# Kernel tuning notes

Hardware: AMD Instinct MI355X
Metric: run time of the kernel (lower is better)

## Reference

```python
import jax, jax.numpy as jnp
import numpy as np

B, S, D, H = 2, 2048, 1024, 16
HD = D // H
SCALE = HD ** -0.5


def setup_inputs() -> dict:
    key = jax.random.key(0)
    ks = jax.random.split(key, 9)
    w = 0.02
    return {
        "query": jax.random.normal(ks[0], (B, S, D), jnp.float32),
        "key": jax.random.normal(ks[1], (B, S, D), jnp.float32),
        "value": jax.random.normal(ks[2], (B, S, D), jnp.float32),
        # precomputed structural bias matrix B_struct [B, S, S]
        "bias_struct": jax.random.uniform(ks[3], (B, S, S), jnp.float32, 0.0, 1.5),
        "Wq": jax.random.normal(ks[4], (D, D), jnp.float32) * w,
        "bq": jnp.zeros((D,), jnp.float32),
        "Wk": jax.random.normal(ks[5], (D, D), jnp.float32) * w,
        "bk": jnp.zeros((D,), jnp.float32),
        "Wv": jax.random.normal(ks[6], (D, D), jnp.float32) * w,
        "bv": jnp.zeros((D,), jnp.float32),
        "Wo": jax.random.normal(ks[7], (D, D), jnp.float32) * w,
        "bo": jnp.zeros((D,), jnp.float32),
        "lambda_bias": jnp.array(1.0, jnp.float32),
    }


def _split_heads(x):
    # [B, S, D] -> [B, H, S, HD]
    b, s, _ = x.shape
    return x.reshape(b, s, H, HD).transpose(0, 2, 1, 3)


def reference(query, key, value, bias_struct, Wq, bq, Wk, bk, Wv, bv, Wo, bo, lambda_bias):
    # Linear projections (torch Linear: x @ W.T + b)
    Q = _split_heads(query @ Wq.T + bq)
    K = _split_heads(key @ Wk.T + bk)
    V = _split_heads(value @ Wv.T + bv)
    # scores = QK^T * scale + lambda * B_struct (broadcast over heads)
    scores = jnp.einsum("bhqd,bhkd->bhqk", Q, K) * SCALE
    scores = scores + lambda_bias * bias_struct[:, None, :, :]
    attn = jax.nn.softmax(scores, axis=-1)
    out = jnp.einsum("bhqk,bhkd->bhqd", attn, V)
    out = out.transpose(0, 2, 1, 3).reshape(query.shape[0], query.shape[1], D)
    return out @ Wo.T + bo
```

## Files before the change

kernel.cpp:

```cpp
#include <hip/hip_runtime.h>
#include <hip/hip_bf16.h>

namespace {

constexpr int B  = 2;
constexpr int S  = 2048;
constexpr int D  = 1024;
constexpr int H  = 16;
constexpr float SCALE = 0.125f;

constexpr int GM = B * S;
constexpr int GN = D;
constexpr int GK = D;

typedef __bf16 bf16x8 __attribute__((ext_vector_type(8)));
typedef float  f32x4  __attribute__((ext_vector_type(4)));
typedef unsigned short u16;
typedef u16 u16x8 __attribute__((ext_vector_type(8)));
typedef u16 u16x4 __attribute__((ext_vector_type(4)));

__device__ __forceinline__ u16 f2bf(float f) {
  union { float f; unsigned u; } v{f};
  unsigned r = v.u + 0x7fffu + ((v.u >> 16) & 1u);
  return (u16)(r >> 16);
}

__device__ __forceinline__ f32x4 mfma16(bf16x8 a, bf16x8 b, f32x4 c) {
  return __builtin_amdgcn_mfma_f32_16x16x32_bf16(a, b, c, 0, 0, 0);
}

__device__ __forceinline__ void gload_lds16(const u16* g, u16* l) {
  __builtin_amdgcn_global_load_lds(
      (const __attribute__((address_space(1))) void*)g,
      (__attribute__((address_space(3))) void*)l, 16, 0, 0);
}

__global__ __launch_bounds__(256) void cvt3_k(
    const float* __restrict__ a, const float* __restrict__ b,
    const float* __restrict__ c, u16* __restrict__ da,
    u16* __restrict__ db, u16* __restrict__ dc)
{
  const float* s = (blockIdx.z == 0) ? a : (blockIdx.z == 1) ? b : c;
  u16* d = (blockIdx.z == 0) ? da : (blockIdx.z == 1) ? db : dc;
  size_t i = ((size_t)blockIdx.x * 256 + threadIdx.x) * 4;
  float4 v = *(const float4*)&s[i];
  u16x4 o = { f2bf(v.x), f2bf(v.y), f2bf(v.z), f2bf(v.w) };
  *(u16x4*)&d[i] = o;
}

__global__ __launch_bounds__(256) void cvt4_k(
    const float* __restrict__ a, const float* __restrict__ b,
    const float* __restrict__ c, const float* __restrict__ e,
    u16* __restrict__ da, u16* __restrict__ db,
    u16* __restrict__ dc, u16* __restrict__ de)
{
  const float* s = (blockIdx.z == 0) ? a : (blockIdx.z == 1) ? b
                 : (blockIdx.z == 2) ? c : e;
  u16* d = (blockIdx.z == 0) ? da : (blockIdx.z == 1) ? db
         : (blockIdx.z == 2) ? dc : de;
  size_t i = ((size_t)blockIdx.x * 256 + threadIdx.x) * 4;
  float4 v = *(const float4*)&s[i];
  u16x4 o = { f2bf(v.x), f2bf(v.y), f2bf(v.z), f2bf(v.w) };
  *(u16x4*)&d[i] = o;
}

template <bool OUTBF, int NZ>
__global__ __launch_bounds__(256) void gemm128_k(
    const u16* __restrict__ A0, const u16* __restrict__ W0, const float* __restrict__ bias0,
    const u16* __restrict__ A1, const u16* __restrict__ W1, const float* __restrict__ bias1,
    u16* __restrict__ Cb0, u16* __restrict__ Cb1, float* __restrict__ Cf)
{
  __shared__ u16 Al[2][128 * 64];
  __shared__ u16 Bl[2][128 * 64];

  const int z = (NZ > 1) ? blockIdx.z : 0;
  const u16* Ap = (z == 0) ? A0 : A1;
  const u16* Wp = (z == 0) ? W0 : W1;
  const float* bias = (z == 0) ? bias0 : bias1;
  u16* Cb = (z == 0) ? Cb0 : Cb1;

  const int tid  = threadIdx.x;
  const int lane = tid & 63;
  const int w    = tid >> 6;
  const int wr = w >> 1, wc = w & 1;
  const int lg = lane >> 4, ll = lane & 15;
  const int bm = blockIdx.y * 128, bn = blockIdx.x * 128;

  auto STAGE = [&](int buf, int k0) {
#pragma unroll
    for (int i = 0; i < 4; ++i) {
      const int c   = (w * 4 + i) * 64 + lane;
      const int row = c >> 3, cs = c & 7;
      const int dofs = ((cs * 16) ^ ((row & 7) << 4)) >> 1;
      gload_lds16(&Ap[(size_t)(bm + row) * GK + k0 + dofs],
                  &Al[buf][(w * 4 + i) * 512]);
      gload_lds16(&Wp[(size_t)(bn + row) * GK + k0 + dofs],
                  &Bl[buf][(w * 4 + i) * 512]);
    }
  };

  f32x4 acc[4][4] = {};

  STAGE(0, 0);
  __syncthreads();

  int cur = 0;
  constexpr int NT = GK / 64;
  for (int t = 0; t < NT; ++t) {
    if (t + 1 < NT) STAGE(cur ^ 1, (t + 1) * 64);
#pragma unroll
    for (int half = 0; half < 2; ++half) {
      bf16x8 af[4], bfr[4];
#pragma unroll
      for (int mi = 0; mi < 4; ++mi) {
        const int row = wr * 64 + mi * 16 + ll;
        af[mi] = *(const bf16x8*)&Al[cur][row * 64 +
                   (((half * 64 + lg * 16) ^ ((row & 7) << 4)) >> 1)];
      }
#pragma unroll
      for (int ni = 0; ni < 4; ++ni) {
        const int row = wc * 64 + ni * 16 + ll;
        bfr[ni] = *(const bf16x8*)&Bl[cur][row * 64 +
                   (((half * 64 + lg * 16) ^ ((row & 7) << 4)) >> 1)];
      }
#pragma unroll
      for (int mi = 0; mi < 4; ++mi)
#pragma unroll
        for (int ni = 0; ni < 4; ++ni)
          acc[mi][ni] = mfma16(af[mi], bfr[ni], acc[mi][ni]);
    }
    __syncthreads();
    cur ^= 1;
  }

#pragma unroll
  for (int ni = 0; ni < 4; ++ni) {
    const int gcol = bn + wc * 64 + ni * 16 + ll;
    const float bv = bias[gcol];
#pragma unroll
    for (int mi = 0; mi < 4; ++mi) {
      const int grow = bm + wr * 64 + mi * 16 + lg * 4;
#pragma unroll
      for (int r = 0; r < 4; ++r) {
        float v = acc[mi][ni][r] + bv;
        if (OUTBF) Cb[(size_t)(grow + r) * GN + gcol] = f2bf(v);
        else       Cf[(size_t)(grow + r) * GN + gcol] = v;
      }
    }
  }
}

__global__ __launch_bounds__(256) void transpose_v_k(
    const u16* __restrict__ Vb, u16* __restrict__ Vt)
{
  __shared__ u16 T[64][72];
  const int tid = threadIdx.x;
  const int bh = blockIdx.y, b = bh >> 4, h = bh & 15;
  const int s0 = blockIdx.x * 64;
#pragma unroll
  for (int it = 0; it < 2; ++it) {
    int idx = tid + it * 256;
    int s = idx >> 3, dc = idx & 7;
    *(uint4*)&T[s][dc * 8] =
        *(const uint4*)&Vb[(size_t)(b * S + s0 + s) * D + h * 64 + dc * 8];
  }
  __syncthreads();
#pragma unroll
  for (int it = 0; it < 2; ++it) {
    int idx = tid + it * 256;
    int d = idx >> 3, sc = idx & 7;
    u16x8 o;
#pragma unroll
    for (int jj = 0; jj < 8; ++jj) o[jj] = T[sc * 8 + jj][d];
    *(u16x8*)&Vt[((size_t)bh * 64 + d) * S + s0 + sc * 8] = o;
  }
}

__global__ __launch_bounds__(256, 3) void attn_mfma2_k(
    const u16* __restrict__ Qb, const u16* __restrict__ Kb,
    const u16* __restrict__ Vt, const float* __restrict__ biasS,
    const float* __restrict__ lamp, u16* __restrict__ Ob)
{
  __shared__ u16 Kl[2][64 * 64];
  __shared__ u16 Pl[4][16][72];

  const int tid  = threadIdx.x;
  const int lane = tid & 63;
  const int w    = tid >> 6;
  const int lg = lane >> 4, ll = lane & 15;
  const int bh = blockIdx.y, b = bh >> 4, h = bh & 15;
  const int qw = blockIdx.x * 64 + w * 16;
  const float lam = lamp[0];

  bf16x8 aQ[2];
  {
    const u16* qrow = &Qb[(size_t)(b * S + qw + ll) * D + h * 64];
    aQ[0] = *(const bf16x8*)&qrow[lg * 8];
    aQ[1] = *(const bf16x8*)&qrow[32 + lg * 8];
  }

  const u16* Kbase = &Kb[(size_t)(b * S) * D + h * 64];
  const u16* Vbase = &Vt[(size_t)bh * 64 * S];
  const float* Bb  = &biasS[((size_t)b * S + qw + lg * 4) * S];

  auto STAGE_K = [&](int buf, int k0) {
#pragma unroll
    for (int i = 0; i < 2; ++i) {
      const int c   = (w * 2 + i) * 64 + lane;
      const int row = c >> 3, cs = c & 7;
      const int dofs = ((cs * 16) ^ ((row & 7) << 4)) >> 1;
      gload_lds16(&Kbase[(size_t)(k0 + row) * D + dofs],
                  &Kl[buf][(w * 2 + i) * 512]);
    }
  };

  f32x4 accO[4] = {};
  float m_r[4], l_r[4];
#pragma unroll
  for (int r = 0; r < 4; ++r) { m_r[r] = -1e30f; l_r[r] = 0.f; }

  float bc[4][4];
  STAGE_K(0, 0);
#pragma unroll
  for (int r = 0; r < 4; ++r)
#pragma unroll
    for (int kf = 0; kf < 4; ++kf)
      bc[r][kf] = Bb[(size_t)r * S + kf * 16 + ll];
  __syncthreads();

  int cur = 0;
  constexpr int NT = S / 64;
  for (int t = 0; t < NT; ++t) {
    const int k0 = t * 64;
    if (t + 1 < NT) STAGE_K(cur ^ 1, k0 + 64);

    bf16x8 v0[4], v1[4];
#pragma unroll
    for (int nf = 0; nf < 4; ++nf) {
      const u16* vrow = &Vbase[(size_t)(nf * 16 + ll) * S + k0];
      v0[nf] = *(const bf16x8*)&vrow[lg * 8];
      v1[nf] = *(const bf16x8*)&vrow[32 + lg * 8];
    }
    float bn[4][4];
    if (t + 1 < NT) {
#pragma unroll
      for (int r = 0; r < 4; ++r)
#pragma unroll
        for (int kf = 0; kf < 4; ++kf)
          bn[r][kf] = Bb[(size_t)r * S + k0 + 64 + kf * 16 + ll];
    }

    f32x4 sf[4];
#pragma unroll
    for (int kf = 0; kf < 4; ++kf) {
      const int row = kf * 16 + ll;
      const u16* kr = &Kl[cur][row * 64];
      bf16x8 kb0 = *(const bf16x8*)&kr[((lg * 16) ^ ((row & 7) << 4)) >> 1];
      bf16x8 kb1 = *(const bf16x8*)&kr[((64 + lg * 16) ^ ((row & 7) << 4)) >> 1];
      f32x4 t4 = {0.f, 0.f, 0.f, 0.f};
      t4 = mfma16(aQ[0], kb0, t4);
      t4 = mfma16(aQ[1], kb1, t4);
#pragma unroll
      for (int r = 0; r < 4; ++r)
        t4[r] = t4[r] * SCALE + lam * bc[r][kf];
      sf[kf] = t4;
    }

#pragma unroll
    for (int r = 0; r < 4; ++r) {
      float pm = fmaxf(fmaxf(sf[0][r], sf[1][r]), fmaxf(sf[2][r], sf[3][r]));
      pm = fmaxf(pm, __shfl_xor(pm, 1));
      pm = fmaxf(pm, __shfl_xor(pm, 2));
      pm = fmaxf(pm, __shfl_xor(pm, 4));
      pm = fmaxf(pm, __shfl_xor(pm, 8));
      float nm = fmaxf(m_r[r], pm);
      float cf = __expf(m_r[r] - nm);
      m_r[r] = nm;
      float ps = 0.f;
#pragma unroll
      for (int kf = 0; kf < 4; ++kf) {
        float p = __expf(sf[kf][r] - nm);
        Pl[w][lg * 4 + r][kf * 16 + ll] = f2bf(p);
        ps += p;
      }
      ps += __shfl_xor(ps, 1);
      ps += __shfl_xor(ps, 2);
      ps += __shfl_xor(ps, 4);
      ps += __shfl_xor(ps, 8);
      l_r[r] = l_r[r] * cf + ps;
#pragma unroll
      for (int nf = 0; nf < 4; ++nf) accO[nf][r] *= cf;
    }

    bf16x8 aP0 = *(const bf16x8*)&Pl[w][ll][lg * 8];
    bf16x8 aP1 = *(const bf16x8*)&Pl[w][ll][32 + lg * 8];
#pragma unroll
    for (int nf = 0; nf < 4; ++nf) {
      accO[nf] = mfma16(aP0, v0[nf], accO[nf]);
      accO[nf] = mfma16(aP1, v1[nf], accO[nf]);
    }

    if (t + 1 < NT) {
#pragma unroll
      for (int r = 0; r < 4; ++r)
#pragma unroll
        for (int kf = 0; kf < 4; ++kf) bc[r][kf] = bn[r][kf];
    }
    __syncthreads();
    cur ^= 1;
  }

  float inv[4];
#pragma unroll
  for (int r = 0; r < 4; ++r) inv[r] = 1.0f / l_r[r];
#pragma unroll
  for (int nf = 0; nf < 4; ++nf)
#pragma unroll
    for (int r = 0; r < 4; ++r)
      Ob[(size_t)(b * S + qw + lg * 4 + r) * D + h * 64 + nf * 16 + ll] =
          f2bf(accO[nf][r] * inv[r]);
}

}

extern "C" void kernel_launch(void* const* d_in, const int* in_sizes, int n_in,
                              void* d_out, int out_size, void* d_ws, size_t ws_size,
                              hipStream_t stream)
{
  const float* query = (const float*)d_in[0];
  const float* key   = (const float*)d_in[1];
  const float* value = (const float*)d_in[2];
  const float* biasS = (const float*)d_in[3];
  const float* Wq = (const float*)d_in[4];
  const float* bq = (const float*)d_in[5];
  const float* Wk = (const float*)d_in[6];
  const float* bk = (const float*)d_in[7];
  const float* Wv = (const float*)d_in[8];
  const float* bv = (const float*)d_in[9];
  const float* Wo = (const float*)d_in[10];
  const float* bo = (const float*)d_in[11];
  const float* lam = (const float*)d_in[12];
  float* out = (float*)d_out;

  char* ws = (char*)d_ws;
  const size_t MB = 1024 * 1024;
  u16* Xq  = (u16*)(ws + 0 * MB);
  u16* Xk  = (u16*)(ws + 8 * MB);
  u16* Xv  = (u16*)(ws + 16 * MB);
  u16* WqB = (u16*)(ws + 24 * MB);
  u16* WkB = (u16*)(ws + 26 * MB);
  u16* WvB = (u16*)(ws + 28 * MB);
  u16* WoB = (u16*)(ws + 30 * MB);
  u16* Qbf = (u16*)(ws + 32 * MB);
  u16* Kbf = (u16*)(ws + 40 * MB);
  u16* Vbf = Xq;
  u16* Vt  = Xk;
  u16* Obf = Xv;

  cvt3_k<<<dim3(4096, 1, 3), 256, 0, stream>>>(query, key, value, Xq, Xk, Xv);
  cvt4_k<<<dim3(1024, 1, 4), 256, 0, stream>>>(Wq, Wk, Wv, Wo, WqB, WkB, WvB, WoB);

  dim3 pgrid(GN / 128, GM / 128, 2);
  gemm128_k<true, 2><<<pgrid, 256, 0, stream>>>(
      Xq, WqB, bq, Xk, WkB, bk, Qbf, Kbf, nullptr);
  dim3 vgrid(GN / 128, GM / 128, 1);
  gemm128_k<true, 1><<<vgrid, 256, 0, stream>>>(
      Xv, WvB, bv, nullptr, nullptr, nullptr, Vbf, nullptr, nullptr);

  transpose_v_k<<<dim3(S / 64, B * H), 256, 0, stream>>>(Vbf, Vt);

  attn_mfma2_k<<<dim3(S / 64, B * H), 256, 0, stream>>>(Qbf, Kbf, Vt, biasS, lam, Obf);

  gemm128_k<false, 1><<<vgrid, 256, 0, stream>>>(
      Obf, WoB, bo, nullptr, nullptr, nullptr, nullptr, nullptr, out);
}
```

Before: 364.1 us.

## Split attention over two KV halves with merge kernel; fuse QKV GEMMs

Result: slower. 888.5 us (+144.0%).

```diff
diff --git a/kernel.cpp b/kernel.cpp
--- a/kernel.cpp
+++ b/kernel.cpp
@@ -7,7 +7,9 @@
 constexpr int S  = 2048;
 constexpr int D  = 1024;
 constexpr int H  = 16;
+constexpr int BH = B * H;
 constexpr float SCALE = 0.125f;
+constexpr float THR = 8.0f;
 
 constexpr int GM = B * S;
 constexpr int GN = D;
@@ -23,6 +25,10 @@
   union { float f; unsigned u; } v{f};
   unsigned r = v.u + 0x7fffu + ((v.u >> 16) & 1u);
   return (u16)(r >> 16);
+}
+__device__ __forceinline__ float bf2f(u16 u) {
+  union { unsigned u; float f; } v{(unsigned)u << 16};
+  return v.f;
 }
 
 __device__ __forceinline__ f32x4 mfma16(bf16x8 a, bf16x8 b, f32x4 c) {
@@ -65,52 +71,59 @@
 }
 
 template <bool OUTBF, int NZ>
-__global__ __launch_bounds__(256) void gemm128_k(
-    const u16* __restrict__ A0, const u16* __restrict__ W0, const float* __restrict__ bias0,
-    const u16* __restrict__ A1, const u16* __restrict__ W1, const float* __restrict__ bias1,
-    u16* __restrict__ Cb0, u16* __restrict__ Cb1, float* __restrict__ Cf)
-{
-  __shared__ u16 Al[2][128 * 64];
-  __shared__ u16 Bl[2][128 * 64];
+__global__ __launch_bounds__(256) void gemm_k(
+    const u16* __restrict__ A0, const u16* __restrict__ A1, const u16* __restrict__ A2,
+    const u16* __restrict__ W0, const u16* __restrict__ W1, const u16* __restrict__ W2,
+    const float* __restrict__ b0, const float* __restrict__ b1, const float* __restrict__ b2,
+    u16* __restrict__ C0, u16* __restrict__ C1, u16* __restrict__ C2,
+    float* __restrict__ Cf)
+{
+  constexpr int BM = 128, BN = 64, BK = 64;
+  __shared__ u16 Al[2][BM * BK];
+  __shared__ u16 Bl[2][BN * BK];
 
   const int z = (NZ > 1) ? blockIdx.z : 0;
-  const u16* Ap = (z == 0) ? A0 : A1;
-  const u16* Wp = (z == 0) ? W0 : W1;
-  const float* bias = (z == 0) ? bias0 : bias1;
-  u16* Cb = (z == 0) ? Cb0 : Cb1;
+  const u16* Ap = (z == 0) ? A0 : (z == 1) ? A1 : A2;
+  const u16* Wp = (z == 0) ? W0 : (z == 1) ? W1 : W2;
+  const float* bias = (z == 0) ? b0 : (z == 1) ? b1 : b2;
+  u16* Cb = (z == 0) ? C0 : (z == 1) ? C1 : C2;
 
   const int tid  = threadIdx.x;
   const int lane = tid & 63;
   const int w    = tid >> 6;
   const int wr = w >> 1, wc = w & 1;
   const int lg = lane >> 4, ll = lane & 15;
-  const int bm = blockIdx.y * 128, bn = blockIdx.x * 128;
+  const int bm = blockIdx.y * BM, bn = blockIdx.x * BN;
 
   auto STAGE = [&](int buf, int k0) {
 #pragma unroll
     for (int i = 0; i < 4; ++i) {
-      const int c   = (w * 4 + i) * 64 + lane;
+      const int c = i * 256 + tid;
       const int row = c >> 3, cs = c & 7;
       const int dofs = ((cs * 16) ^ ((row & 7) << 4)) >> 1;
-      gload_lds16(&Ap[(size_t)(bm + row) * GK + k0 + dofs],
-                  &Al[buf][(w * 4 + i) * 512]);
-      gload_lds16(&Wp[(size_t)(bn + row) * GK + k0 + dofs],
-                  &Bl[buf][(w * 4 + i) * 512]);
+      gload_lds16(&Ap[(size_t)(bm + row) * GK + k0 + dofs], &Al[buf][c * 8]);
+    }
+#pragma unroll
+    for (int i = 0; i < 2; ++i) {
+      const int c = i * 256 + tid;
+      const int row = c >> 3, cs = c & 7;
+      const int dofs = ((cs * 16) ^ ((row & 7) << 4)) >> 1;
+      gload_lds16(&Wp[(size_t)(bn + row) * GK + k0 + dofs], &Bl[buf][c * 8]);
     }
   };
 
-  f32x4 acc[4][4] = {};
+  f32x4 acc[4][2] = {};
 
   STAGE(0, 0);
   __syncthreads();
 
   int cur = 0;
-  constexpr int NT = GK / 64;
+  constexpr int NT = GK / BK;
   for (int t = 0; t < NT; ++t) {
-    if (t + 1 < NT) STAGE(cur ^ 1, (t + 1) * 64);
+    if (t + 1 < NT) STAGE(cur ^ 1, (t + 1) * BK);
 #pragma unroll
     for (int half = 0; half < 2; ++half) {
-      bf16x8 af[4], bfr[4];
+      bf16x8 af[4], bfr[2];
 #pragma unroll
       for (int mi = 0; mi < 4; ++mi) {
         const int row = wr * 64 + mi * 16 + ll;
@@ -118,15 +131,15 @@
                    (((half * 64 + lg * 16) ^ ((row & 7) << 4)) >> 1)];
       }
 #pragma unroll
-      for (int ni = 0; ni < 4; ++ni) {
-        const int row = wc * 64 + ni * 16 + ll;
+      for (int ni = 0; ni < 2; ++ni) {
+        const int row = wc * 32 + ni * 16 + ll;
         bfr[ni] = *(const bf16x8*)&Bl[cur][row * 64 +
                    (((half * 64 + lg * 16) ^ ((row & 7) << 4)) >> 1)];
       }
 #pragma unroll
       for (int mi = 0; mi < 4; ++mi)
 #pragma unroll
-        for (int ni = 0; ni < 4; ++ni)
+        for (int ni = 0; ni < 2; ++ni)
           acc[mi][ni] = mfma16(af[mi], bfr[ni], acc[mi][ni]);
     }
     __syncthreads();
@@ -134,8 +147,8 @@
   }
 
 #pragma unroll
-  for (int ni = 0; ni < 4; ++ni) {
-    const int gcol = bn + wc * 64 + ni * 16 + ll;
+  for (int ni = 0; ni < 2; ++ni) {
+    const int gcol = bn + wc * 32 + ni * 16 + ll;
     const float bv = bias[gcol];
 #pragma unroll
     for (int mi = 0; mi < 4; ++mi) {
@@ -176,13 +189,14 @@
   }
 }
 
-__global__ __launch_bounds__(256, 3) void attn_mfma2_k(
+__global__ __launch_bounds__(256, 6) void attn_split_k(
     const u16* __restrict__ Qb, const u16* __restrict__ Kb,
     const u16* __restrict__ Vt, const float* __restrict__ biasS,
-    const float* __restrict__ lamp, u16* __restrict__ Ob)
+    const float* __restrict__ lamp, u16* __restrict__ Opart,
+    float2* __restrict__ Ml)
 {
   __shared__ u16 Kl[2][64 * 64];
-  __shared__ u16 Pl[4][16][72];
+  __shared__ __bf16 Pl[4][16][72];
 
   const int tid  = threadIdx.x;
   const int lane = tid & 63;
@@ -190,6 +204,8 @@
   const int lg = lane >> 4, ll = lane & 15;
   const int bh = blockIdx.y, b = bh >> 4, h = bh & 15;
   const int qw = blockIdx.x * 64 + w * 16;
+  const int split = blockIdx.z;
+  const int kvbase = split * (S / 2);
   const float lam = lamp[0];
 
   bf16x8 aQ[2];
@@ -199,9 +215,9 @@
     aQ[1] = *(const bf16x8*)&qrow[32 + lg * 8];
   }
 
-  const u16* Kbase = &Kb[(size_t)(b * S) * D + h * 64];
-  const u16* Vbase = &Vt[(size_t)bh * 64 * S];
-  const float* Bb  = &biasS[((size_t)b * S + qw + lg * 4) * S];
+  const u16* Kbase = &Kb[(size_t)(b * S + kvbase) * D + h * 64];
+  const u16* Vbase = &Vt[(size_t)bh * 64 * S + kvbase];
+  const float* Bb  = &biasS[((size_t)b * S + qw + lg * 4) * S + kvbase];
 
   auto STAGE_K = [&](int buf, int k0) {
 #pragma unroll
@@ -229,7 +245,7 @@
   __syncthreads();
 
   int cur = 0;
-  constexpr int NT = S / 64;
+  constexpr int NT = (S / 2) / 64;
   for (int t = 0; t < NT; ++t) {
     const int k0 = t * 64;
     if (t + 1 < NT) STAGE_K(cur ^ 1, k0 + 64);
@@ -241,13 +257,13 @@
       v0[nf] = *(const bf16x8*)&vrow[lg * 8];
       v1[nf] = *(const bf16x8*)&vrow[32 + lg * 8];
     }
-    float bn[4][4];
+    float bnx[4][4];
     if (t + 1 < NT) {
 #pragma unroll
       for (int r = 0; r < 4; ++r)
 #pragma unroll
         for (int kf = 0; kf < 4; ++kf)
-          bn[r][kf] = Bb[(size_t)r * S + k0 + 64 + kf * 16 + ll];
+          bnx[r][kf] = Bb[(size_t)r * S + k0 + 64 + kf * 16 + ll];
     }
 
     f32x4 sf[4];
@@ -266,30 +282,38 @@
       sf[kf] = t4;
     }
 
+    float pm[4];
+#pragma unroll
+    for (int r = 0; r < 4; ++r)
+      pm[r] = fmaxf(fmaxf(sf[0][r], sf[1][r]), fmaxf(sf[2][r], sf[3][r]));
+    float ex = fmaxf(fmaxf(pm[0] - m_r[0], pm[1] - m_r[1]),
+                     fmaxf(pm[2] - m_r[2], pm[3] - m_r[3]));
+    if (__any(ex > THR)) {
+#pragma unroll
+      for (int r = 0; r < 4; ++r) {
+        float tmx = pm[r];
+        tmx = fmaxf(tmx, __shfl_xor(tmx, 1));
+        tmx = fmaxf(tmx, __shfl_xor(tmx, 2));
+        tmx = fmaxf(tmx, __shfl_xor(tmx, 4));
+        tmx = fmaxf(tmx, __shfl_xor(tmx, 8));
+        float nm = fmaxf(m_r[r], tmx);
+        float cf = __expf(m_r[r] - nm);
+        m_r[r] = nm;
+        l_r[r] *= cf;
+#pragma unroll
+        for (int nf = 0; nf < 4; ++nf) accO[nf][r] *= cf;
+      }
+    }
 #pragma unroll
     for (int r = 0; r < 4; ++r) {
-      float pm = fmaxf(fmaxf(sf[0][r], sf[1][r]), fmaxf(sf[2][r], sf[3][r]));
-      pm = fmaxf(pm, __shfl_xor(pm, 1));
-      pm = fmaxf(pm, __shfl_xor(pm, 2));
-      pm = fmaxf(pm, __shfl_xor(pm, 4));
-      pm = fmaxf(pm, __shfl_xor(pm, 8));
-      float nm = fmaxf(m_r[r], pm);
-      float cf = __expf(m_r[r] - nm);
-      m_r[r] = nm;
       float ps = 0.f;
 #pragma unroll
       for (int kf = 0; kf < 4; ++kf) {
-        float p = __expf(sf[kf][r] - nm);
-        Pl[w][lg * 4 + r][kf * 16 + ll] = f2bf(p);
+        float p = __expf(sf[kf][r] - m_r[r]);
+        Pl[w][lg * 4 + r][kf * 16 + ll] = (__bf16)p;
         ps += p;
       }
-      ps += __shfl_xor(ps, 1);
-      ps += __shfl_xor(ps, 2);
-      ps += __shfl_xor(ps, 4);
-      ps += __shfl_xor(ps, 8);
-      l_r[r] = l_r[r] * cf + ps;
-#pragma unroll
-      for (int nf = 0; nf < 4; ++nf) accO[nf][r] *= cf;
+      l_r[r] += ps;
     }
 
     bf16x8 aP0 = *(const bf16x8*)&Pl[w][ll][lg * 8];
@@ -304,21 +328,60 @@
 #pragma unroll
       for (int r = 0; r < 4; ++r)
 #pragma unroll
-        for (int kf = 0; kf < 4; ++kf) bc[r][kf] = bn[r][kf];
+        for (int kf = 0; kf < 4; ++kf) bc[r][kf] = bnx[r][kf];
     }
     __syncthreads();
     cur ^= 1;
   }
 
-  float inv[4];
-#pragma unroll
-  for (int r = 0; r < 4; ++r) inv[r] = 1.0f / l_r[r];
+#pragma unroll
+  for (int r = 0; r < 4; ++r) {
+    float tl = l_r[r];
+    tl += __shfl_xor(tl, 1);
+    tl += __shfl_xor(tl, 2);
+    tl += __shfl_xor(tl, 4);
+    tl += __shfl_xor(tl, 8);
+    l_r[r] = tl;
+  }
+
+  u16* Op = Opart + (size_t)split * ((size_t)BH * S * 64);
+  float2* Mlp = Ml + (size_t)split * ((size_t)BH * S);
+  if (ll == 0) {
+#pragma unroll
+    for (int r = 0; r < 4; ++r) {
+      float2 v; v.x = m_r[r]; v.y = l_r[r];
+      Mlp[(size_t)bh * S + qw + lg * 4 + r] = v;
+    }
+  }
 #pragma unroll
   for (int nf = 0; nf < 4; ++nf)
 #pragma unroll
     for (int r = 0; r < 4; ++r)
-      Ob[(size_t)(b * S + qw + lg * 4 + r) * D + h * 64 + nf * 16 + ll] =
-          f2bf(accO[nf][r] * inv[r]);
+      Op[((size_t)bh * S + qw + lg * 4 + r) * 64 + nf * 16 + ll] =
+          f2bf(accO[nf][r]);
+}
+
+__global__ __launch_bounds__(256) void merge_k(
+    const u16* __restrict__ Opart, const float2* __restrict__ Ml,
+    u16* __restrict__ Obf)
+{
+  const int tid = threadIdx.x;
+  const size_t row = (size_t)blockIdx.x * 32 + (tid >> 3);
+  const int dc = (tid & 7) * 8;
+  const float2 ml0 = Ml[row];
+  const float2 ml1 = Ml[(size_t)BH * S + row];
+  const float m = fmaxf(ml0.x, ml1.x);
+  float c0 = __expf(ml0.x - m), c1 = __expf(ml1.x - m);
+  const float inv = 1.0f / (c0 * ml0.y + c1 * ml1.y);
+  c0 *= inv; c1 *= inv;
+  u16x8 a = *(const u16x8*)&Opart[row * 64 + dc];
+  u16x8 bq = *(const u16x8*)&Opart[(size_t)BH * S * 64 + row * 64 + dc];
+  u16x8 o;
+#pragma unroll
+  for (int j = 0; j < 8; ++j)
+    o[j] = f2bf(c0 * bf2f(a[j]) + c1 * bf2f(bq[j]));
+  const int bh = (int)(row >> 11), q = (int)(row & 2047);
+  *(u16x8*)&Obf[((size_t)((bh >> 4) * S + q)) * D + (bh & 15) * 64 + dc] = o;
 }
 
 }
@@ -353,24 +416,28 @@
   u16* WoB = (u16*)(ws + 30 * MB);
   u16* Qbf = (u16*)(ws + 32 * MB);
   u16* Kbf = (u16*)(ws + 40 * MB);
-  u16* Vbf = Xq;
-  u16* Vt  = Xk;
-  u16* Obf = Xv;
+  u16* Opart = (u16*)ws;
+  u16* Obf   = (u16*)(ws + 16 * MB);
+  u16* Vbf = (u16*)d_out;
+  u16* Vt  = (u16*)d_out + (size_t)4 * MB;
+  float2* Ml = (float2*)d_out;
 
   cvt3_k<<<dim3(4096, 1, 3), 256, 0, stream>>>(query, key, value, Xq, Xk, Xv);
   cvt4_k<<<dim3(1024, 1, 4), 256, 0, stream>>>(Wq, Wk, Wv, Wo, WqB, WkB, WvB, WoB);
 
-  dim3 pgrid(GN / 128, GM / 128, 2);
-  gemm128_k<true, 2><<<pgrid, 256, 0, stream>>>(
-      Xq, WqB, bq, Xk, WkB, bk, Qbf, Kbf, nullptr);
-  dim3 vgrid(GN / 128, GM / 128, 1);
-  gemm128_k<true, 1><<<vgrid, 256, 0, stream>>>(
-      Xv, WvB, bv, nullptr, nullptr, nullptr, Vbf, nullptr, nullptr);
+  dim3 pgrid(GN / 64, GM / 128, 3);
+  gemm_k<true, 3><<<pgrid, 256, 0, stream>>>(
+      Xq, Xk, Xv, WqB, WkB, WvB, bq, bk, bv, Qbf, Kbf, Vbf, nullptr);
 
   transpose_v_k<<<dim3(S / 64, B * H), 256, 0, stream>>>(Vbf, Vt);
 
-  attn_mfma2_k<<<dim3(S / 64, B * H), 256, 0, stream>>>(Qbf, Kbf, Vt, biasS, lam, Obf);
-
-  gemm128_k<false, 1><<<vgrid, 256, 0, stream>>>(
-      Obf, WoB, bo, nullptr, nullptr, nullptr, nullptr, nullptr, out);
-}
+  attn_split_k<<<dim3(S / 64, BH, 2), 256, 0, stream>>>(
+      Qbf, Kbf, Vt, biasS, lam, Opart, Ml);
+
+  merge_k<<<dim3(BH * S / 32), 256, 0, stream>>>(Opart, Ml, Obf);
+
+  dim3 ogrid(GN / 64, GM / 128, 1);
+  gemm_k<false, 1><<<ogrid, 256, 0, stream>>>(
+      Obf, nullptr, nullptr, WoB, nullptr, nullptr, bo, nullptr, nullptr,
+      nullptr, nullptr, nullptr, out);
+}
```
